# Kernel optimization log

Hardware: AMD Instinct MI355X
Metric: run time of the kernel (lower is better)

## Reference

```python
import jax, jax.numpy as jnp
import numpy as np

NEG = -1e9  # large negative used as log(0) to keep grads finite
EPS = 1e-38


def _pcfg_inside(theta_log, Phi):
    # theta_log: [N,N,N] (A -> B C), Phi: [B,N,T] log terminal probs
    B, N, T = Phi.shape
    tm = jnp.max(theta_log)
    et = jnp.exp(theta_log - tm)  # [A,Bn,Cn], all > 0
    beta = jnp.full((B, N, T, T), NEG, dtype=Phi.dtype)
    idx = jnp.arange(T)
    beta = beta.at[:, :, idx, idx].set(Phi)  # length-1 spans
    for l in range(2, T + 1):
        P = T - l + 1
        ii = jnp.arange(P)
        ss = jnp.arange(l - 1)
        lcol = ii[:, None] + ss[None, :]          # left child end  [P,S]
        left = beta[:, :, ii[:, None], lcol]      # [B,N,P,S]
        right = beta[:, :, lcol + 1, (ii + l - 1)[:, None]]  # [B,N,P,S]
        ml = jnp.max(left, axis=1)                # [B,P,S]
        mr = jnp.max(right, axis=1)
        el = jnp.exp(left - ml[:, None])
        er = jnp.exp(right - mr[:, None])
        inner = jnp.einsum('xyz,byps,bzps->bxps', et, el, er)
        sc = jnp.log(jnp.maximum(inner, EPS)) + tm + ml[:, None] + mr[:, None]
        score = jax.scipy.special.logsumexp(sc, axis=-1)  # over split points -> [B,N,P]
        beta = beta.at[:, :, ii, ii + l - 1].set(score)
    logZ = beta[:, 0, 0, T - 1]  # start symbol id 0, full span
    return beta, logZ


def _pcfg_outside(theta_log, beta):
    B, N, T, _ = beta.shape
    tm = jnp.max(theta_log)
    et = jnp.exp(theta_log - tm)
    alpha = jnp.full((B, N, T, T), NEG, dtype=beta.dtype)
    alpha = alpha.at[:, 0, 0, T - 1].set(0.0)
    for l in range(T, 1, -1):  # parent spans, longest first
        P = T - l + 1
        ii = jnp.arange(P)
        jj = ii + l - 1
        ss = jnp.arange(l - 1)
        lcol = ii[:, None] + ss[None, :]          # left child end  [P,S]
        rrow = lcol + 1                            # right child start
        a = alpha[:, :, ii, jj]                    # [B,N,P]
        lb = beta[:, :, ii[:, None], lcol]         # [B,N,P,S]
        rb = beta[:, :, rrow, jj[:, None]]         # [B,N,P,S]
        ma = jnp.max(a, axis=1)                    # [B,P]
        ea = jnp.exp(a - ma[:, None])
        mrb = jnp.max(rb, axis=1)
        erb = jnp.exp(rb - mrb[:, None])
        mlb = jnp.max(lb, axis=1)
        elb = jnp.exp(lb - mlb[:, None])
        cL = jnp.log(jnp.maximum(jnp.einsum('xyz,bxp,bzps->byps', et, ea, erb), EPS)) \
             + tm + ma[:, None, :, None] + mrb[:, None]
        cR = jnp.log(jnp.maximum(jnp.einsum('xyz,bxp,byps->bzps', et, ea, elb), EPS)) \
             + tm + ma[:, None, :, None] + mlb[:, None]
        alpha = alpha.at[:, :, ii[:, None], lcol].set(
            jnp.logaddexp(alpha[:, :, ii[:, None], lcol], cL))
        alpha = alpha.at[:, :, rrow, jj[:, None]].set(
            jnp.logaddexp(alpha[:, :, rrow, jj[:, None]], cR))
    return alpha


def setup_inputs() -> dict:
    key = jax.random.key(0)
    ks = jax.random.split(key, 6)
    B, T, k, N, V = 16, 32, 512, 24, 32000
    g_seq = jax.random.normal(ks[0], (B, T, k), dtype=jnp.float32)
    Theta = jax.random.normal(ks[1], (N, N, N), dtype=jnp.float32) * 0.01
    nt2vocab = (jax.random.uniform(ks[2], (N, V), dtype=jnp.float32) < 0.05).astype(jnp.float32)
    ln_gamma = jnp.ones((k,), jnp.float32)
    ln_beta = jnp.zeros((k,), jnp.float32)
    W1 = jax.random.normal(ks[3], (k, 128), dtype=jnp.float32) * 0.02
    b1 = jnp.zeros((128,), jnp.float32)
    W2 = jax.random.normal(ks[4], (128, N), dtype=jnp.float32) * 0.02
    b2 = jnp.zeros((N,), jnp.float32)
    return {"g_seq": g_seq, "Theta": Theta, "nt2vocab": nt2vocab,
            "ln_gamma": ln_gamma, "ln_beta": ln_beta,
            "W1": W1, "b1": b1, "W2": W2, "b2": b2}


def reference(g_seq, Theta, nt2vocab, ln_gamma, ln_beta, W1, b1, W2, b2):
    # term head: LayerNorm -> Linear(k,128) -> GELU(exact) -> Linear(128,N)
    mu = jnp.mean(g_seq, axis=-1, keepdims=True)
    var = jnp.var(g_seq, axis=-1, keepdims=True)  # biased, as torch LayerNorm
    g = (g_seq - mu) / jnp.sqrt(var + 1e-5) * ln_gamma + ln_beta
    h = jax.nn.gelu(g @ W1 + b1, approximate=False)
    out = h @ W2 + b2                                # [B,T,N]
    Phi = jax.nn.log_softmax(out.transpose(0, 2, 1), axis=1)   # [B,N,T]
    theta_log = jax.nn.log_softmax(Theta, axis=-1)   # softmax over flattened (B,C) last dim == axis -1 of [N,N,N] after view(-1,N)
    N = Theta.shape[0]
    theta_log = jax.nn.log_softmax(Theta.reshape(-1, N), axis=-1).reshape(N, N, N)
    beta, logZ = _pcfg_inside(theta_log, Phi)
    alpha = _pcfg_outside(theta_log, beta)
    T = Phi.shape[2]
    idx = jnp.arange(T)
    p_nt = jnp.exp(alpha[:, :, idx, idx] + beta[:, :, idx, idx] - logZ[:, None, None])  # [B,N,T]
    mask_logits = jnp.log(1e-6 + jnp.einsum('bnt,nv->btv', p_nt, nt2vocab))
    L_pcfg = (-logZ).mean()
    return mask_logits, L_pcfg
```

## Files before the change

kernel.cpp:

```cpp
#include <hip/hip_runtime.h>
#include <math.h>

#define NEGV -1000000000.0f
#define EPSV 1e-38f
#define SENTU 0x7FC00001u

typedef _Float16 h16;
typedef _Float16 h2 __attribute__((ext_vector_type(2)));
typedef _Float16 h4 __attribute__((ext_vector_type(4)));

constexpr int BSTRIDE = 528 * 32;
constexpr int ASTRIDE = 528 * 24;

constexpr int O_WK   = 28032;
constexpr int O_EA   = 28032;
constexpr int O_EBF  = 31008;
constexpr int O_EB16 = 33984;
constexpr int O_RR   = 35472;
constexpr int O_EA24 = 36656;
constexpr int O_MRL  = 37424;
constexpr int O_MSM  = 37552;
constexpr int O_SCAL = 37680;
constexpr int SMEM_SZ = 37744;

__device__ __forceinline__ int tri(int i, int j) { return ((j * (j + 1)) >> 1) + i; }
__device__ __forceinline__ float la2(float a, float c) {
  float mx = fmaxf(a, c), mn = fminf(a, c);
  return mx + log1pf(__expf(mn - mx));
}
__device__ __forceinline__ void gstore(float* p, float v) {
  __hip_atomic_store(p, v, __ATOMIC_RELAXED, __HIP_MEMORY_SCOPE_AGENT);
}
__device__ __forceinline__ float gload(const float* p) {
  return __hip_atomic_load(p, __ATOMIC_RELAXED, __HIP_MEMORY_SCOPE_AGENT);
}
__device__ __forceinline__ void storeu(unsigned* p, unsigned v) {
  __hip_atomic_store(p, v, __ATOMIC_RELAXED, __HIP_MEMORY_SCOPE_AGENT);
}
__device__ __forceinline__ unsigned loadu(const unsigned* p) {
  return __hip_atomic_load(p, __ATOMIC_RELAXED, __HIP_MEMORY_SCOPE_AGENT);
}
__device__ __forceinline__ float d2(h16 ax, h16 ay, h16 bx, h16 by, float c) {
#if __has_builtin(__builtin_amdgcn_fdot2)
  h2 a; a.x = ax; a.y = ay;
  h2 b; b.x = bx; b.y = by;
  return __builtin_amdgcn_fdot2(a, b, c, false);
#else
  return c + (float)ax * (float)bx + (float)ay * (float)by;
#endif
}
__device__ __forceinline__ float wmax64(float v) {
#pragma unroll
  for (int off = 32; off; off >>= 1) v = fmaxf(v, __shfl_xor(v, off));
  return v;
}

#define MAX12(A, B, C)                                                        \
  fmaxf(fmaxf(fmaxf(fmaxf(A.x, A.y), fmaxf(A.z, A.w)),                        \
              fmaxf(fmaxf(B.x, B.y), fmaxf(B.z, B.w))),                       \
        fmaxf(fmaxf(C.x, C.y), fmaxf(C.z, C.w)))

__global__ void __launch_bounds__(256, 2) mega_kernel(
    const float* __restrict__ g_seq, const float* __restrict__ Theta,
    const float* __restrict__ vocab, const float* __restrict__ lng,
    const float* __restrict__ lnb, const float* __restrict__ W1,
    const float* __restrict__ bb1, const float* __restrict__ W2,
    const float* __restrict__ bb2, float* __restrict__ out,
    float* __restrict__ et_g, float* __restrict__ beta_g,
    float* __restrict__ aL_g, float* __restrict__ aR_g,
    unsigned* __restrict__ cnt, float* __restrict__ logZg) {
  __shared__ __align__(16) unsigned char smem[SMEM_SZ];
  h16* et16h = (h16*)smem;
  float* wk = (float*)(smem + O_WK);
  const int tid = threadIdx.x;
  const int blk = blockIdx.x;
  const int b = blk & 15, local = blk >> 4;
  unsigned* gcnt  = cnt;
  unsigned* done  = cnt + 8;
  unsigned* ibc   = cnt + 16 + b * 16;
  unsigned* slotO = cnt + 512 + b * 64 + 32;
  float* bbase = beta_g + b * BSTRIDE;
  float* aLb = aL_g + b * ASTRIDE;
  float* aRb = aR_g + b * ASTRIDE;

  {
    float* g = wk;
    float2* red = (float2*)(wk + 512);
    float* hb = wk + 1024;
    float* ob = wk + 1152;
    float* sc = wk + 1184;
    float2 raw = ((const float2*)(g_seq + (size_t)blk * 512))[tid];
    red[tid] = make_float2(raw.x + raw.y, raw.x * raw.x + raw.y * raw.y);
    __syncthreads();
    if (tid < 128) { float2 o = red[tid + 128], m = red[tid]; red[tid] = make_float2(m.x + o.x, m.y + o.y); }
    __syncthreads();
    if (tid < 64) {
      float2 v = red[tid], o = red[tid + 64];
      v.x += o.x; v.y += o.y;
      for (int off = 32; off; off >>= 1) { v.x += __shfl_xor(v.x, off); v.y += __shfl_xor(v.y, off); }
      if (tid == 0) {
        float mu = v.x / 512.0f;
        float var = v.y / 512.0f - mu * mu;
        sc[0] = mu; sc[1] = rsqrtf(var + 1e-5f);
      }
    }
    __syncthreads();
    float mu = sc[0], rstd = sc[1];
    g[2 * tid]     = (raw.x - mu) * rstd * lng[2 * tid]     + lnb[2 * tid];
    g[2 * tid + 1] = (raw.y - mu) * rstd * lng[2 * tid + 1] + lnb[2 * tid + 1];
    __syncthreads();
    {
      int j = tid & 127, hh = tid >> 7, c0 = hh * 256;
      float a0 = 0, a1 = 0, a2 = 0, a3 = 0;
      for (int c = 0; c < 256; c += 4) {
        a0 = fmaf(g[c0 + c],     W1[(c0 + c) * 128 + j],     a0);
        a1 = fmaf(g[c0 + c + 1], W1[(c0 + c + 1) * 128 + j], a1);
        a2 = fmaf(g[c0 + c + 2], W1[(c0 + c + 2) * 128 + j], a2);
        a3 = fmaf(g[c0 + c + 3], W1[(c0 + c + 3) * 128 + j], a3);
      }
      ((float*)red)[tid] = (a0 + a1) + (a2 + a3);
    }
    __syncthreads();
    if (tid < 128) {
      float a = ((float*)red)[tid] + ((float*)red)[tid + 128] + bb1[tid];
      hb[tid] = 0.5f * a * (1.0f + erff(a * 0.70710678118654752f));
    }
    __syncthreads();
    if (tid < 192) {
      int n = tid >> 3, q = tid & 7;
      float a = 0;
      for (int k = 0; k < 16; k++) a = fmaf(hb[q * 16 + k], W2[(q * 16 + k) * 24 + n], a);
      ((float*)red)[tid] = a;
    }
    __syncthreads();
    if (tid < 24) {
      float a = bb2[tid];
      for (int q = 0; q < 8; q++) a += ((float*)red)[tid * 8 + q];
      ob[tid] = a;
    }
    __syncthreads();
    if (tid == 0) {
      float m = ob[0];
      for (int n = 1; n < 24; n++) m = fmaxf(m, ob[n]);
      float s = 0;
      for (int n = 0; n < 24; n++) s += __expf(ob[n] - m);
      sc[2] = m + __logf(s);
    }
    __syncthreads();
    if (tid < 24) {
      int fb = blk >> 5, ft = blk & 31;
      gstore(beta_g + (size_t)fb * BSTRIDE + tri(ft, ft) * 32 + tid, ob[tid] - sc[2]);
    }
  }
  if (tid < 64) {
    int z = tid & 31;
    bool up = tid >= 32;
    int row = up ? (512 + blk) : blk;
    bool valid = (!up) || (blk < 64);
    float v = (z < 24 && valid) ? Theta[row * 24 + z] : NEGV;
    float m = v;
    for (int off = 16; off; off >>= 1) m = fmaxf(m, __shfl_xor(m, off));
    float e = (z < 24 && valid) ? __expf(v - m) : 0.f;
    float s = e;
    for (int off = 16; off; off >>= 1) s += __shfl_xor(s, off);
    float lse = m + __logf(s);
    if (z < 24 && valid) gstore(et_g + row * 24 + z, __expf(v - lse));
  }
  for (int idx = blk * 256 + tid; idx < 2 * 16 * ASTRIDE; idx += 131072) {
    float v = NEGV;
    if (idx < 16 * ASTRIDE && (idx % ASTRIDE) == 11904) v = 0.f;
    gstore(aL_g + idx, v);
  }
  for (int idx = blk * 256 + tid; idx < 16 * BSTRIDE; idx += 131072) {
    int w = idx % BSTRIDE;
    int cell = w >> 5, wic = w & 31;
    if (wic >= 24) continue;
    int t0 = (int)((sqrtf(8.f * (float)cell + 9.f) - 3.f) * 0.5f + 0.5f);
    bool isDiag = false;
#pragma unroll
    for (int dt = -1; dt <= 1; ++dt) {
      int t = t0 + dt;
      if (t >= 0 && ((t * (t + 3)) >> 1) == cell) isDiag = true;
    }
    if (!isDiag) gstore(beta_g + idx, __uint_as_float(SENTU));
  }
  __builtin_amdgcn_s_waitcnt(0);
  __syncthreads();
  if (tid == 0) {
    __hip_atomic_fetch_add(ibc, 1u, __ATOMIC_RELAXED, __HIP_MEMORY_SCOPE_AGENT);
    if (local == 0) {
      while (loadu(ibc) < 32u) __builtin_amdgcn_s_sleep(2);
      __hip_atomic_fetch_add(gcnt, 1u, __ATOMIC_RELAXED, __HIP_MEMORY_SCOPE_AGENT);
    }
    while (loadu(gcnt) < 16u) __builtin_amdgcn_s_sleep(2);
  }
  __syncthreads();

  for (int i4 = tid; i4 < 3456; i4 += 256) {
    int f = i4 * 4;
    int x = f / 576, r = f - x * 576;
    float4 v = ((const float4*)et_g)[i4];
    h4 t; t.x = (h16)v.x; t.y = (h16)v.y; t.z = (h16)v.z; t.w = (h16)v.w;
    *(h4*)(et16h + x * 584 + r) = t;
  }
  __syncthreads();

  {
    float* eA   = (float*)(smem + O_EA);
    float* eBf  = (float*)(smem + O_EBF);
    h16*  eb16  = (h16*)(smem + O_EB16);
    h16*  rrh   = (h16*)(smem + O_RR);
    float* mrl  = (float*)(smem + O_MRL);
    float* scal = (float*)(smem + O_SCAL);
    const int lastLI = 32 - local;
    for (int l = 2; l <= lastLI; l++) {
      int S = l - 1;
      int i = local, j = i + S, SN = S * 24;
      for (int idx4 = tid; idx4 < 6 * S; idx4 += 256) {
        int s = idx4 / 6, q = idx4 - 6 * s;
        ((float4*)eA)[idx4] = ((const float4*)(bbase + (size_t)tri(i, i + s) * 32))[q];
        const float* cp = bbase + (size_t)tri(i + s + 1, j) * 32 + q * 4;
        float w0 = gload(cp), w1 = gload(cp + 1), w2 = gload(cp + 2), w3 = gload(cp + 3);
        while ((__float_as_uint(w0) == SENTU) | (__float_as_uint(w1) == SENTU) |
               (__float_as_uint(w2) == SENTU) | (__float_as_uint(w3) == SENTU)) {
          __builtin_amdgcn_s_sleep(1);
          w0 = gload(cp); w1 = gload(cp + 1); w2 = gload(cp + 2); w3 = gload(cp + 3);
        }
        float4 t4; t4.x = w0; t4.y = w1; t4.z = w2; t4.w = w3;
        ((float4*)eBf)[idx4] = t4;
      }
      __syncthreads();
      if (tid < 64) {
        int s = tid >> 1, h12 = tid & 1;
        float pa = NEGV, pb = NEGV;
        if (s < S) {
          const float4* ra = (const float4*)(eA + s * 24 + h12 * 12);
          float4 A = ra[0], B = ra[1], C = ra[2];
          pa = MAX12(A, B, C);
          const float4* rb = (const float4*)(eBf + s * 24 + h12 * 12);
          float4 D = rb[0], E = rb[1], F = rb[2];
          pb = MAX12(D, E, F);
        }
        pa = fmaxf(pa, __shfl_xor(pa, 1));
        pb = fmaxf(pb, __shfl_xor(pb, 1));
        if (s < S && h12 == 0) mrl[s] = pb;
        float M0 = wmax64((s < S) ? pa + pb : NEGV);
        if (tid == 0) scal[0] = M0;
      }
      __syncthreads();
      float M = scal[0];
      for (int idx = tid; idx < SN; idx += 256) {
        int s = idx / 24;
        float m_ = mrl[s];
        eA[idx] = __expf(eA[idx] + m_ - M);
        eb16[idx] = (h16)__expf(eBf[idx] - m_);
      }
      __syncthreads();
      if (tid < 144) {
        int y = tid / 6, zq = tid % 6;
        float4 acc = make_float4(0, 0, 0, 0);
        for (int s = 0; s < S; s++) {
          float a = eA[s * 24 + y];
          h4 b4 = ((const h4*)(eb16 + s * 24))[zq];
          acc.x = fmaf(a, (float)b4.x, acc.x); acc.y = fmaf(a, (float)b4.y, acc.y);
          acc.z = fmaf(a, (float)b4.z, acc.z); acc.w = fmaf(a, (float)b4.w, acc.w);
        }
        h4 t; t.x = (h16)acc.x; t.y = (h16)acc.y; t.z = (h16)acc.z; t.w = (h16)acc.w;
        ((h4*)(rrh + y * 24))[zq] = t;
      }
      __syncthreads();
      if (tid < 48) {
        int x = tid >> 1, hh = tid & 1;
        const h4* ep = (const h4*)(et16h + x * 584 + hh * 288);
        const h4* rp = (const h4*)(rrh + hh * 288);
        float a2 = 0.f;
#pragma unroll 8
        for (int q = 0; q < 72; ++q) {
          h4 ev = ep[q], rv = rp[q];
          a2 = d2(ev.x, ev.y, rv.x, rv.y, a2);
          a2 = d2(ev.z, ev.w, rv.z, rv.w, a2);
        }
        a2 += __shfl_xor(a2, 1);
        if (hh == 0)
          gstore(bbase + (size_t)tri(i, j) * 32 + x, M + __logf(fmaxf(a2, EPSV)));
      }
      __builtin_amdgcn_s_waitcnt(0);
      __syncthreads();
    }
  }
  if (local == 0 && tid == 0) {
    gstore(logZg + b, gload(bbase + 496 * 32));
    __builtin_amdgcn_s_waitcnt(0);
    __hip_atomic_fetch_add(done, 1u, __ATOMIC_RELAXED, __HIP_MEMORY_SCOPE_AGENT);
  }

  {
    float* ebL  = (float*)(smem + O_EA);
    float* ebRf = (float*)(smem + O_EBF);
    h16*  eb16  = (h16*)(smem + O_EB16);
    h16*  rrh   = (h16*)(smem + O_RR);
    float* ea24 = (float*)(smem + O_EA24);
    float* mLs  = (float*)(smem + O_MRL);
    float* mRs  = (float*)(smem + O_MSM);
    float* scal = (float*)(smem + O_SCAL);
    const int lastLO = 32 - local;
    for (int l = lastLO; l >= 2; l--) {
      int S = l - 1;
      int i = local, j = i + S, SN = S * 24;
      if (local > 0 && tid == 0) {
        unsigned need = (unsigned)(32 - l);
        while (loadu(slotO + local - 1) < need) __builtin_amdgcn_s_sleep(1);
      }
      __builtin_amdgcn_s_waitcnt(0);
      __syncthreads();
      if (tid < 64) {
        float av = NEGV;
        if (tid < 24)
          av = la2(gload(aLb + tri(i, j) * 24 + tid), gload(aRb + tri(i, j) * 24 + tid));
        float mav = wmax64(av);
        if (tid < 24) ea24[tid] = __expf(av - mav);
        if (tid == 0) scal[0] = mav;
      } else {
        for (int idx4 = tid - 64; idx4 < 6 * S; idx4 += 192) {
          int s = idx4 / 6, q = idx4 - 6 * s;
          ((float4*)ebL)[idx4]  = ((const float4*)(bbase + (size_t)tri(i, i + s) * 32))[q];
          ((float4*)ebRf)[idx4] = ((const float4*)(bbase + (size_t)tri(i + s + 1, j) * 32))[q];
        }
      }
      __syncthreads();
      float ma = scal[0];
      if (tid < 64) {
        int s = tid >> 1, h12 = tid & 1;
        float pl = NEGV, pr = NEGV;
        if (s < S) {
          const float4* ra = (const float4*)(ebL + s * 24 + h12 * 12);
          float4 A = ra[0], B = ra[1], C = ra[2];
          pl = MAX12(A, B, C);
          const float4* rb = (const float4*)(ebRf + s * 24 + h12 * 12);
          float4 D = rb[0], E = rb[1], F = rb[2];
          pr = MAX12(D, E, F);
        }
        pl = fmaxf(pl, __shfl_xor(pl, 1));
        pr = fmaxf(pr, __shfl_xor(pr, 1));
        if (s < S && h12 == 0) { mLs[s] = pl; mRs[s] = pr; }
      } else if (tid < 208) {
        int t = tid - 64, y = t / 6, zq = t % 6;
        float4 acc = make_float4(0, 0, 0, 0);
#pragma unroll 4
        for (int x = 0; x < 24; x++) {
          float a = ea24[x];
          h4 ev = ((const h4*)(et16h + x * 584 + y * 24))[zq];
          acc.x = fmaf(a, (float)ev.x, acc.x); acc.y = fmaf(a, (float)ev.y, acc.y);
          acc.z = fmaf(a, (float)ev.z, acc.z); acc.w = fmaf(a, (float)ev.w, acc.w);
        }
        h4 t4; t4.x = (h16)acc.x; t4.y = (h16)acc.y; t4.z = (h16)acc.z; t4.w = (h16)acc.w;
        ((h4*)(rrh + y * 24))[zq] = t4;
      }
      __syncthreads();
      for (int idx = tid; idx < SN; idx += 256) {
        int s = idx / 24;
        ebL[idx] = __expf(ebL[idx] - mLs[s]);
        eb16[idx] = (h16)__expf(ebRf[idx] - mRs[s]);
      }
      __syncthreads();
      for (int u = tid; u < SN; u += 256) {
        int s = u / 24, z = u - s * 24;
        float acc = 0;
        for (int y = 0; y < 24; y++) acc = fmaf((float)rrh[y * 24 + z], ebL[s * 24 + y], acc);
        float val = __logf(fmaxf(acc, EPSV)) + ma + mLs[s];
        float* t = aRb + tri(i + s + 1, j) * 24 + z;
        gstore(t, la2(gload(t), val));
      }
      __builtin_amdgcn_s_waitcnt(0);
      __syncthreads();
      if (tid == 0) storeu(slotO + local, (unsigned)(33 - l));
      for (int u = tid; u < SN; u += 256) {
        int s = u / 24, y = u - s * 24;
        const h4* w4 = (const h4*)(rrh + y * 24);
        const h4* r4 = (const h4*)(eb16 + s * 24);
        float acc = 0;
#pragma unroll
        for (int q = 0; q < 6; q++) {
          h4 a = w4[q], c4 = r4[q];
          acc = d2(a.x, a.y, c4.x, c4.y, acc);
          acc = d2(a.z, a.w, c4.z, c4.w, acc);
        }
        float val = __logf(fmaxf(acc, EPSV)) + ma + mRs[s];
        float* t = aLb + tri(i, i + s) * 24 + y;
        gstore(t, la2(gload(t), val));
      }
    }
    __builtin_amdgcn_s_waitcnt(0);
    __syncthreads();
    if (tid == 0) storeu(slotO + local, 32u);
  }

  {
    int vbase = local * 1000;
    float pv0[24], pv1[24];
    {
      int o0 = tid, o1 = tid + 256;
      bool k0 = o0 < 1000, k1 = o1 < 1000;
#pragma unroll
      for (int n = 0; n < 24; n++) {
        pv0[n] = k0 ? vocab[n * 32000 + vbase + o0] : 0.f;
        pv1[n] = k1 ? vocab[n * 32000 + vbase + o1] : 0.f;
      }
    }
    if (tid < 64) {
      for (;;) {
        unsigned v = 32;
        if (tid < 31) v = loadu(slotO + tid);
        if (__ballot(v >= 32u) == ~0ull) break;
        __builtin_amdgcn_s_sleep(1);
      }
    }
    __syncthreads();
    float* p = (float*)smem;
    float logZv = gload(bbase + 496 * 32);
    for (int c = tid; c < 768; c += 256) {
      int n = c >> 5, t = c & 31;
      int dA = tri(t, t) * 24 + n;
      float al = gload(aLb + dA), ar = gload(aRb + dA);
      p[c] = __expf(la2(al, ar) + bbase[(size_t)tri(t, t) * 32 + n] - logZv);
    }
    __syncthreads();
    for (int pass = 0; pass < 2; pass++) {
      int o0 = tid + pass * 512, o1 = o0 + 256;
      bool v0ok = o0 < 1000, v1ok = o1 < 1000;
      int v0 = vbase + o0, v1 = vbase + o1;
      if (pass == 1) {
#pragma unroll
        for (int n = 0; n < 24; n++) {
          pv0[n] = v0ok ? vocab[n * 32000 + v0] : 0.f;
          pv1[n] = v1ok ? vocab[n * 32000 + v1] : 0.f;
        }
      }
      float* ob0 = out + (size_t)b * 32 * 32000 + v0;
      float* ob1 = out + (size_t)b * 32 * 32000 + v1;
      for (int t4 = 0; t4 < 32; t4 += 4) {
        float a00 = 1e-6f, a01 = 1e-6f, a02 = 1e-6f, a03 = 1e-6f;
        float a10 = 1e-6f, a11 = 1e-6f, a12 = 1e-6f, a13 = 1e-6f;
#pragma unroll 6
        for (int n = 0; n < 24; n++) {
          float4 pv = *(const float4*)(p + n * 32 + t4);
          a00 = fmaf(pv.x, pv0[n], a00); a01 = fmaf(pv.y, pv0[n], a01);
          a02 = fmaf(pv.z, pv0[n], a02); a03 = fmaf(pv.w, pv0[n], a03);
          a10 = fmaf(pv.x, pv1[n], a10); a11 = fmaf(pv.y, pv1[n], a11);
          a12 = fmaf(pv.z, pv1[n], a12); a13 = fmaf(pv.w, pv1[n], a13);
        }
        if (v0ok) {
          ob0[(size_t)(t4 + 0) * 32000] = __logf(a00);
          ob0[(size_t)(t4 + 1) * 32000] = __logf(a01);
          ob0[(size_t)(t4 + 2) * 32000] = __logf(a02);
          ob0[(size_t)(t4 + 3) * 32000] = __logf(a03);
        }
        if (v1ok) {
          ob1[(size_t)(t4 + 0) * 32000] = __logf(a10);
          ob1[(size_t)(t4 + 1) * 32000] = __logf(a11);
          ob1[(size_t)(t4 + 2) * 32000] = __logf(a12);
          ob1[(size_t)(t4 + 3) * 32000] = __logf(a13);
        }
      }
    }
    if (blk == 0 && tid == 0) {
      while (loadu(done) < 16u) __builtin_amdgcn_s_sleep(2);
      float s = 0;
      for (int q = 0; q < 16; q++) s += gload(logZg + q);
      out[16384000] = -s / 16.0f;
    }
  }
}

extern "C" void kernel_launch(void* const* d_in, const int* in_sizes, int n_in,
                              void* d_out, int out_size, void* d_ws, size_t ws_size,
                              hipStream_t stream) {
  (void)in_sizes; (void)n_in; (void)out_size; (void)ws_size;
  const float* g_seq = (const float*)d_in[0];
  const float* Theta = (const float*)d_in[1];
  const float* vocab = (const float*)d_in[2];
  const float* lng   = (const float*)d_in[3];
  const float* lnb   = (const float*)d_in[4];
  const float* W1    = (const float*)d_in[5];
  const float* bb1   = (const float*)d_in[6];
  const float* W2    = (const float*)d_in[7];
  const float* bb2   = (const float*)d_in[8];
  float* out = (float*)d_out;

  float* ws = (float*)d_ws;
  unsigned* cnt = (unsigned*)d_ws;
  float* logZg  = ws + 2048;
  float* et_g   = ws + 4096;
  float* beta_g = ws + 18432;
  float* aL_g   = beta_g + 16 * BSTRIDE;
  float* aR_g   = aL_g + 16 * ASTRIDE;

  hipMemsetAsync(d_ws, 0, 8192, stream);

  void* args[] = {(void*)&g_seq, (void*)&Theta, (void*)&vocab, (void*)&lng,
                  (void*)&lnb, (void*)&W1, (void*)&bb1, (void*)&W2, (void*)&bb2,
                  (void*)&out, (void*)&et_g, (void*)&beta_g, (void*)&aL_g,
                  (void*)&aR_g, (void*)&cnt, (void*)&logZg};
  hipLaunchCooperativeKernel((const void*)mega_kernel, dim3(512), dim3(256),
                             args, 0, stream);
}
```

Before: 439.0 us.

## Keep row-owned beta and left-outside rows in LDS instead of global memory

Each block owns row i of the span chart. Its beta row and its alpha-left accumulations are now kept in shared memory, so they are no longer reloaded from global memory on every span length. Global writes of alpha-left are cut to the final diagonal only, and the global init of the aL array is dropped. The change also removes some s_waitcnt drains and adds a transposed fp32 copy of the rr matrix for the aR contraction. LDS use grows, which may hurt occupancy at 2 blocks per CU, and the spin loop now also waits on slot 31.

```diff
diff --git a/kernel.cpp b/kernel.cpp
--- a/kernel.cpp
+++ b/kernel.cpp
@@ -12,16 +12,19 @@
 constexpr int BSTRIDE = 528 * 32;
 constexpr int ASTRIDE = 528 * 24;
 
-constexpr int O_WK   = 28032;
-constexpr int O_EA   = 28032;
-constexpr int O_EBF  = 31008;
-constexpr int O_EB16 = 33984;
-constexpr int O_RR   = 35472;
-constexpr int O_EA24 = 36656;
-constexpr int O_MRL  = 37424;
-constexpr int O_MSM  = 37552;
-constexpr int O_SCAL = 37680;
-constexpr int SMEM_SZ = 37744;
+constexpr int O_WK    = 28032;
+constexpr int O_BOWN  = 28032;
+constexpr int O_ALOWN = 31104;
+constexpr int O_EA    = 34176;
+constexpr int O_EBF   = 37152;
+constexpr int O_EB16  = 40128;
+constexpr int O_RR    = 41616;
+constexpr int O_WT    = 42800;
+constexpr int O_EA24  = 45200;
+constexpr int O_MRL   = 45296;
+constexpr int O_MSM   = 45424;
+constexpr int O_SCAL  = 45552;
+constexpr int SMEM_SZ = 45616;
 
 __device__ __forceinline__ int tri(int i, int j) { return ((j * (j + 1)) >> 1) + i; }
 __device__ __forceinline__ float la2(float a, float c) {
@@ -72,6 +75,8 @@
   __shared__ __align__(16) unsigned char smem[SMEM_SZ];
   h16* et16h = (h16*)smem;
   float* wk = (float*)(smem + O_WK);
+  float* betaOwn = (float*)(smem + O_BOWN);
+  float* aLOwn   = (float*)(smem + O_ALOWN);
   const int tid = threadIdx.x;
   const int blk = blockIdx.x;
   const int b = blk & 15, local = blk >> 4;
@@ -166,11 +171,8 @@
     float lse = m + __logf(s);
     if (z < 24 && valid) gstore(et_g + row * 24 + z, __expf(v - lse));
   }
-  for (int idx = blk * 256 + tid; idx < 2 * 16 * ASTRIDE; idx += 131072) {
-    float v = NEGV;
-    if (idx < 16 * ASTRIDE && (idx % ASTRIDE) == 11904) v = 0.f;
-    gstore(aL_g + idx, v);
-  }
+  for (int idx = blk * 256 + tid; idx < 16 * ASTRIDE; idx += 131072)
+    gstore(aR_g + idx, NEGV);
   for (int idx = blk * 256 + tid; idx < 16 * BSTRIDE; idx += 131072) {
     int w = idx % BSTRIDE;
     int cell = w >> 5, wic = w & 31;
@@ -203,6 +205,9 @@
     h4 t; t.x = (h16)v.x; t.y = (h16)v.y; t.z = (h16)v.z; t.w = (h16)v.w;
     *(h4*)(et16h + x * 584 + r) = t;
   }
+  for (int c = tid; c < 768; c += 256)
+    aLOwn[c] = (local == 0 && c == 744) ? 0.f : NEGV;
+  if (tid < 24) betaOwn[tid] = gload(bbase + (size_t)tri(local, local) * 32 + tid);
   __syncthreads();
 
   {
@@ -218,7 +223,6 @@
       int i = local, j = i + S, SN = S * 24;
       for (int idx4 = tid; idx4 < 6 * S; idx4 += 256) {
         int s = idx4 / 6, q = idx4 - 6 * s;
-        ((float4*)eA)[idx4] = ((const float4*)(bbase + (size_t)tri(i, i + s) * 32))[q];
         const float* cp = bbase + (size_t)tri(i + s + 1, j) * 32 + q * 4;
         float w0 = gload(cp), w1 = gload(cp + 1), w2 = gload(cp + 2), w3 = gload(cp + 3);
         while ((__float_as_uint(w0) == SENTU) | (__float_as_uint(w1) == SENTU) |
@@ -234,7 +238,7 @@
         int s = tid >> 1, h12 = tid & 1;
         float pa = NEGV, pb = NEGV;
         if (s < S) {
-          const float4* ra = (const float4*)(eA + s * 24 + h12 * 12);
+          const float4* ra = (const float4*)(betaOwn + s * 24 + h12 * 12);
           float4 A = ra[0], B = ra[1], C = ra[2];
           pa = MAX12(A, B, C);
           const float4* rb = (const float4*)(eBf + s * 24 + h12 * 12);
@@ -252,7 +256,7 @@
       for (int idx = tid; idx < SN; idx += 256) {
         int s = idx / 24;
         float m_ = mrl[s];
-        eA[idx] = __expf(eA[idx] + m_ - M);
+        eA[idx] = __expf(betaOwn[idx] + m_ - M);
         eb16[idx] = (h16)__expf(eBf[idx] - m_);
       }
       __syncthreads();
@@ -281,15 +285,17 @@
           a2 = d2(ev.z, ev.w, rv.z, rv.w, a2);
         }
         a2 += __shfl_xor(a2, 1);
-        if (hh == 0)
-          gstore(bbase + (size_t)tri(i, j) * 32 + x, M + __logf(fmaxf(a2, EPSV)));
-      }
-      __builtin_amdgcn_s_waitcnt(0);
+        if (hh == 0) {
+          float val = M + __logf(fmaxf(a2, EPSV));
+          betaOwn[S * 24 + x] = val;
+          gstore(bbase + (size_t)tri(i, j) * 32 + x, val);
+        }
+      }
       __syncthreads();
     }
   }
   if (local == 0 && tid == 0) {
-    gstore(logZg + b, gload(bbase + 496 * 32));
+    gstore(logZg + b, betaOwn[744]);
     __builtin_amdgcn_s_waitcnt(0);
     __hip_atomic_fetch_add(done, 1u, __ATOMIC_RELAXED, __HIP_MEMORY_SCOPE_AGENT);
   }
@@ -299,6 +305,7 @@
     float* ebRf = (float*)(smem + O_EBF);
     h16*  eb16  = (h16*)(smem + O_EB16);
     h16*  rrh   = (h16*)(smem + O_RR);
+    float* wT   = (float*)(smem + O_WT);
     float* ea24 = (float*)(smem + O_EA24);
     float* mLs  = (float*)(smem + O_MRL);
     float* mRs  = (float*)(smem + O_MSM);
@@ -311,19 +318,17 @@
         unsigned need = (unsigned)(32 - l);
         while (loadu(slotO + local - 1) < need) __builtin_amdgcn_s_sleep(1);
       }
-      __builtin_amdgcn_s_waitcnt(0);
       __syncthreads();
       if (tid < 64) {
         float av = NEGV;
         if (tid < 24)
-          av = la2(gload(aLb + tri(i, j) * 24 + tid), gload(aRb + tri(i, j) * 24 + tid));
+          av = la2(aLOwn[S * 24 + tid], gload(aRb + tri(i, j) * 24 + tid));
         float mav = wmax64(av);
         if (tid < 24) ea24[tid] = __expf(av - mav);
         if (tid == 0) scal[0] = mav;
       } else {
         for (int idx4 = tid - 64; idx4 < 6 * S; idx4 += 192) {
           int s = idx4 / 6, q = idx4 - 6 * s;
-          ((float4*)ebL)[idx4]  = ((const float4*)(bbase + (size_t)tri(i, i + s) * 32))[q];
           ((float4*)ebRf)[idx4] = ((const float4*)(bbase + (size_t)tri(i + s + 1, j) * 32))[q];
         }
       }
@@ -333,7 +338,7 @@
         int s = tid >> 1, h12 = tid & 1;
         float pl = NEGV, pr = NEGV;
         if (s < S) {
-          const float4* ra = (const float4*)(ebL + s * 24 + h12 * 12);
+          const float4* ra = (const float4*)(betaOwn + s * 24 + h12 * 12);
           float4 A = ra[0], B = ra[1], C = ra[2];
           pl = MAX12(A, B, C);
           const float4* rb = (const float4*)(ebRf + s * 24 + h12 * 12);
@@ -355,18 +360,25 @@
         }
         h4 t4; t4.x = (h16)acc.x; t4.y = (h16)acc.y; t4.z = (h16)acc.z; t4.w = (h16)acc.w;
         ((h4*)(rrh + y * 24))[zq] = t4;
+        wT[(4 * zq + 0) * 25 + y] = acc.x;
+        wT[(4 * zq + 1) * 25 + y] = acc.y;
+        wT[(4 * zq + 2) * 25 + y] = acc.z;
+        wT[(4 * zq + 3) * 25 + y] = acc.w;
       }
       __syncthreads();
       for (int idx = tid; idx < SN; idx += 256) {
         int s = idx / 24;
-        ebL[idx] = __expf(ebL[idx] - mLs[s]);
+        ebL[idx] = __expf(betaOwn[idx] - mLs[s]);
         eb16[idx] = (h16)__expf(ebRf[idx] - mRs[s]);
       }
       __syncthreads();
       for (int u = tid; u < SN; u += 256) {
         int s = u / 24, z = u - s * 24;
+        const float* wz = wT + z * 25;
+        const float* el = ebL + s * 24;
         float acc = 0;
-        for (int y = 0; y < 24; y++) acc = fmaf((float)rrh[y * 24 + z], ebL[s * 24 + y], acc);
+#pragma unroll 4
+        for (int y = 0; y < 24; y++) acc = fmaf(wz[y], el[y], acc);
         float val = __logf(fmaxf(acc, EPSV)) + ma + mLs[s];
         float* t = aRb + tri(i + s + 1, j) * 24 + z;
         gstore(t, la2(gload(t), val));
@@ -386,10 +398,11 @@
           acc = d2(a.z, a.w, c4.z, c4.w, acc);
         }
         float val = __logf(fmaxf(acc, EPSV)) + ma + mRs[s];
-        float* t = aLb + tri(i, i + s) * 24 + y;
-        gstore(t, la2(gload(t), val));
-      }
-    }
+        aLOwn[s * 24 + y] = la2(aLOwn[s * 24 + y], val);
+      }
+    }
+    __syncthreads();
+    if (tid < 24) gstore(aLb + tri(local, local) * 24 + tid, aLOwn[tid]);
     __builtin_amdgcn_s_waitcnt(0);
     __syncthreads();
     if (tid == 0) storeu(slotO + local, 32u);
@@ -410,7 +423,7 @@
     if (tid < 64) {
       for (;;) {
         unsigned v = 32;
-        if (tid < 31) v = loadu(slotO + tid);
+        if (tid < 32) v = loadu(slotO + tid);
         if (__ballot(v >= 32u) == ~0ull) break;
         __builtin_amdgcn_s_sleep(1);
       }
```

Measured after the change: 421.6 us. -4.0%, faster.
